# Performance work log

Hardware: AMD Instinct MI355X
Metric: run time of the kernel (lower is better)

## Reference

```python
import jax, jax.numpy as jnp
import numpy as np

MARGIN = 0.0
BINS = 10
ALPHA = 0.75
N = 16777216  # 2**24 pairs


def setup_inputs() -> dict:
    key = jax.random.key(0)
    k1, k2, k3 = jax.random.split(key, 3)
    output1 = jax.random.normal(k1, (N,), dtype=jnp.float32)
    output2 = jax.random.normal(k2, (N,), dtype=jnp.float32)
    target = jax.random.randint(k3, (N,), 0, 2, dtype=jnp.int64)
    return {"output1": output1, "output2": output2, "target": target}


def reference(output1, output2, target):
    dtype = output1.dtype
    t = target.astype(dtype)
    diff = output1 - output2
    # MarginRankingLoss(reduction='none'): max(0, -target*(x1-x2) + margin)
    loss = jnp.maximum(0.0, -t * diff + MARGIN)
    # gradient-norm proxy g in (0,1)
    expected_sign = 2.0 * t - 1.0
    g = jax.nn.sigmoid(-diff * expected_sign + MARGIN)
    g_norm = jnp.abs(g)
    edges = jnp.arange(BINS + 1, dtype=dtype) / BINS
    # histogram over BINS bins (fixed small loop over bins, vectorized over N)
    counts = jnp.stack([
        jnp.sum((g_norm >= edges[i]) & (g_norm < edges[i + 1]))
        for i in range(BINS)
    ]).astype(dtype)
    tot = jnp.clip(counts, 1.0)
    w = tot ** (-ALPHA)  # per-bin weight; constant wrt g in the original (.item() detaches)
    w = jax.lax.stop_gradient(w)
    bin_idx = jnp.clip(jnp.floor(g * BINS).astype(jnp.int32), 0, BINS - 1)
    sample_weights = w[bin_idx]
    return jnp.mean(loss * sample_weights)
```

## Files before the change

### kernel.cpp

```cpp
#include <hip/hip_runtime.h>

#define BINS 10
#define ALPHA 0.75f

constexpr int NB    = 2048;
constexpr int NT    = 256;
constexpr int NWV   = NT / 64;
constexpr int ITERS = 8;

__device__ constexpr float LTH[9] = {
    2.19722458f,  1.38629436f,  0.847297861f, 0.405465108f, 0.0f,
   -0.405465108f, -0.847297861f, -1.38629436f, -2.19722458f};

#define GHM_PROC(AX, BX, TX) do {                                    \
    float diff = (AX) - (BX);                                        \
    float nd   = -diff;                                              \
    bool  tt   = (TX) != 0;                                          \
    float u    = tt ? diff : nd;                                     \
    float loss = tt ? fmaxf(nd, 0.0f) : 0.0f;                        \
    cls[0] += loss;                                                  \
    _Pragma("unroll")                                                \
    for (int k = 1; k < BINS; ++k) {                                 \
      bool p = (u <= LTH[k - 1]);                                    \
      cls[k] += p ? loss : 0.0f;                                     \
      cnt[k] += (unsigned int)p;                                     \
    }                                                                \
  } while (0)

#define GHM_PROC4(AV, BV, TV) do {                                   \
    GHM_PROC((AV).x, (BV).x, (TV).x);                                \
    GHM_PROC((AV).y, (BV).y, (TV).y);                                \
    GHM_PROC((AV).z, (BV).z, (TV).z);                                \
    GHM_PROC((AV).w, (BV).w, (TV).w);                                \
  } while (0)

__device__ __forceinline__ void gl_lds16(const void* g, void* l) {
  __builtin_amdgcn_global_load_lds(
      (const __attribute__((address_space(1))) unsigned int*)g,
      (__attribute__((address_space(3))) unsigned int*)l, 16, 0, 0);
}

__global__ __launch_bounds__(NT) void ghm_pass1(
    const float* __restrict__ o1f, const float* __restrict__ o2f,
    const int* __restrict__ tgt, double* __restrict__ gls,
    unsigned int* __restrict__ gcnt, int n)
{
  const float4* o1 = reinterpret_cast<const float4*>(o1f);
  const float4* o2 = reinterpret_cast<const float4*>(o2f);
  const int4*   tg = reinterpret_cast<const int4*>(tgt);

  float        cls[BINS];
  unsigned int cnt[BINS];
#pragma unroll
  for (int b = 0; b < BINS; ++b) { cls[b] = 0.0f; cnt[b] = 0u; }

  const int lane = threadIdx.x & 63;
  const int wv   = threadIdx.x >> 6;

  __shared__ float4 La[3][NWV][64];
  __shared__ float4 Lb[3][NWV][64];
  __shared__ int4   Lt[3][NWV][64];

  if (n == NB * NT * ITERS * 4 && gridDim.x == NB) {
    const int gbase = blockIdx.x * (NT * ITERS);

#define STAGE(K, BUF) do {                                            \
      const int gi = gbase + (K) * NT + (int)threadIdx.x;             \
      gl_lds16(&o1[gi], &La[BUF][wv][0]);                             \
      gl_lds16(&o2[gi], &Lb[BUF][wv][0]);                             \
      gl_lds16(&tg[gi], &Lt[BUF][wv][0]);                             \
    } while (0)

    STAGE(0, 0);
    STAGE(1, 1);

#pragma unroll
    for (int k = 0; k < ITERS; ++k) {
      if (k == ITERS - 1) asm volatile("s_waitcnt vmcnt(0)" ::: "memory");
      else                asm volatile("s_waitcnt vmcnt(3)" ::: "memory");
      const int buf = k % 3;
      float4 a = La[buf][wv][lane];
      float4 b = Lb[buf][wv][lane];
      int4   t = Lt[buf][wv][lane];
      if (k + 2 < ITERS) { STAGE(k + 2, (k + 2) % 3); }
      GHM_PROC4(a, b, t);
    }
#undef STAGE
  } else {
    const int tid = blockIdx.x * NT + threadIdx.x;
    const int stride = gridDim.x * NT;
    const int n4 = n >> 2;
    for (int i = tid; i < n4; i += stride) {
      float4 a  = o1[i];
      float4 bb = o2[i];
      int4   t  = tg[i];
      GHM_PROC4(a, bb, t);
    }
    if (tid == 0) {
      for (int i = n4 * 4; i < n; ++i) GHM_PROC(o1f[i], o2f[i], tgt[i]);
    }
  }

  __shared__ float        s_ls[NWV][BINS];
  __shared__ unsigned int s_c [NWV][BINS];
#pragma unroll
  for (int b = 0; b < BINS; ++b) {
    float v = cls[b];
    unsigned int cv = cnt[b];
#pragma unroll
    for (int off = 32; off >= 1; off >>= 1) {
      v  += __shfl_down(v, off, 64);
      cv += __shfl_down(cv, off, 64);
    }
    if (lane == 0) { s_ls[wv][b] = v; s_c[wv][b] = cv; }
  }
  __syncthreads();
  if (threadIdx.x < BINS) {
    float v = 0.0f; unsigned int cv = 0u;
#pragma unroll
    for (int w = 0; w < NWV; ++w) { v += s_ls[w][threadIdx.x]; cv += s_c[w][threadIdx.x]; }
    atomicAdd(&gls[threadIdx.x], (double)v);
    if (cv) atomicAdd(&gcnt[threadIdx.x], cv);
  }
}

__global__ void ghm_final(const double* __restrict__ gls,
                          const unsigned int* __restrict__ gcnt,
                          float* __restrict__ out, int n)
{
  if (threadIdx.x == 0) {
    double             CLS[BINS + 1];
    unsigned long long CC [BINS + 1];
#pragma unroll
    for (int b = 0; b < BINS; ++b) { CLS[b] = gls[b]; CC[b] = gcnt[b]; }
    CLS[BINS] = 0.0; CC[BINS] = 0ull;
    CC[0] = (unsigned long long)n;

    double total = 0.0;
#pragma unroll
    for (int b = 0; b < BINS; ++b) {
      double lsb            = CLS[b] - CLS[b + 1];
      unsigned long long cb = CC[b] - CC[b + 1];
      float cf  = (float)cb;
      float tot = fmaxf(cf, 1.0f);
      float wgt = powf(tot, -ALPHA);
      total += lsb * (double)wgt;
    }
    out[0] = (float)(total / (double)n);
  }
}

extern "C" void kernel_launch(void* const* d_in, const int* in_sizes, int n_in,
                              void* d_out, int out_size, void* d_ws, size_t ws_size,
                              hipStream_t stream) {
  const float* o1  = (const float*)d_in[0];
  const float* o2  = (const float*)d_in[1];
  const int*   tgt = (const int*)d_in[2];
  float* out = (float*)d_out;
  const int n = in_sizes[0];

  double*       gls  = (double*)d_ws;
  unsigned int* gcnt = (unsigned int*)((char*)d_ws + BINS * sizeof(double));
  hipMemsetAsync(d_ws, 0, BINS * (sizeof(double) + sizeof(unsigned int)), stream);

  ghm_pass1<<<NB, NT, 0, stream>>>(o1, o2, tgt, gls, gcnt, n);
  ghm_final<<<1, 64, 0, stream>>>(gls, gcnt, out, n);
}
```

Baseline: 218.7 us.

## Replace LDS-staged global loads with register-prefetched nontemporal vector loads

Drops the triple-buffered global_load_lds staging through shared memory. The kernel now prefetches two iterations ahead into registers using nontemporal 128-bit loads, with a sched_barrier to keep the loads issued ahead of the compute. The grid doubles to 4096 blocks and iterations per thread halve to 4, keeping the fast-path size check consistent with 2^24 elements. This removes the LDS round trip and the manual vmcnt waits, at the cost of more live registers per thread and more blocks, each doing less work.

After: 259.0 us. 1.18x slower.

```diff
diff --git a/kernel.cpp b/kernel.cpp
--- a/kernel.cpp
+++ b/kernel.cpp
@@ -3,10 +3,12 @@
 #define BINS 10
 #define ALPHA 0.75f
 
-constexpr int NB    = 2048;
+constexpr int NB    = 4096;
 constexpr int NT    = 256;
-constexpr int NWV   = NT / 64;
-constexpr int ITERS = 8;
+constexpr int ITERS = 4;
+
+typedef float v4f __attribute__((ext_vector_type(4)));
+typedef int   v4i __attribute__((ext_vector_type(4)));
 
 __device__ constexpr float LTH[9] = {
     2.19722458f,  1.38629436f,  0.847297861f, 0.405465108f, 0.0f,
@@ -34,66 +36,47 @@
     GHM_PROC((AV).w, (BV).w, (TV).w);                                \
   } while (0)
 
-__device__ __forceinline__ void gl_lds16(const void* g, void* l) {
-  __builtin_amdgcn_global_load_lds(
-      (const __attribute__((address_space(1))) unsigned int*)g,
-      (__attribute__((address_space(3))) unsigned int*)l, 16, 0, 0);
-}
+__device__ __forceinline__ v4f nt4f(const v4f* p) { return __builtin_nontemporal_load(p); }
+__device__ __forceinline__ v4i nt4i(const v4i* p) { return __builtin_nontemporal_load(p); }
 
 __global__ __launch_bounds__(NT) void ghm_pass1(
     const float* __restrict__ o1f, const float* __restrict__ o2f,
     const int* __restrict__ tgt, double* __restrict__ gls,
     unsigned int* __restrict__ gcnt, int n)
 {
-  const float4* o1 = reinterpret_cast<const float4*>(o1f);
-  const float4* o2 = reinterpret_cast<const float4*>(o2f);
-  const int4*   tg = reinterpret_cast<const int4*>(tgt);
+  const v4f* o1 = reinterpret_cast<const v4f*>(o1f);
+  const v4f* o2 = reinterpret_cast<const v4f*>(o2f);
+  const v4i* tg = reinterpret_cast<const v4i*>(tgt);
 
   float        cls[BINS];
   unsigned int cnt[BINS];
 #pragma unroll
   for (int b = 0; b < BINS; ++b) { cls[b] = 0.0f; cnt[b] = 0u; }
 
-  const int lane = threadIdx.x & 63;
-  const int wv   = threadIdx.x >> 6;
-
-  __shared__ float4 La[3][NWV][64];
-  __shared__ float4 Lb[3][NWV][64];
-  __shared__ int4   Lt[3][NWV][64];
-
   if (n == NB * NT * ITERS * 4 && gridDim.x == NB) {
-    const int gbase = blockIdx.x * (NT * ITERS);
-
-#define STAGE(K, BUF) do {                                            \
-      const int gi = gbase + (K) * NT + (int)threadIdx.x;             \
-      gl_lds16(&o1[gi], &La[BUF][wv][0]);                             \
-      gl_lds16(&o2[gi], &Lb[BUF][wv][0]);                             \
-      gl_lds16(&tg[gi], &Lt[BUF][wv][0]);                             \
-    } while (0)
-
-    STAGE(0, 0);
-    STAGE(1, 1);
-
+    const int base = blockIdx.x * (NT * ITERS) + threadIdx.x;
+    v4f a0 = nt4f(o1 + base);      v4f b0 = nt4f(o2 + base);      v4i t0 = nt4i(tg + base);
+    v4f a1 = nt4f(o1 + base + NT); v4f b1 = nt4f(o2 + base + NT); v4i t1 = nt4i(tg + base + NT);
 #pragma unroll
-    for (int k = 0; k < ITERS; ++k) {
-      if (k == ITERS - 1) asm volatile("s_waitcnt vmcnt(0)" ::: "memory");
-      else                asm volatile("s_waitcnt vmcnt(3)" ::: "memory");
-      const int buf = k % 3;
-      float4 a = La[buf][wv][lane];
-      float4 b = Lb[buf][wv][lane];
-      int4   t = Lt[buf][wv][lane];
-      if (k + 2 < ITERS) { STAGE(k + 2, (k + 2) % 3); }
-      GHM_PROC4(a, b, t);
+    for (int k = 0; k < ITERS - 2; ++k) {
+      v4f a2 = nt4f(o1 + base + (k + 2) * NT);
+      v4f b2 = nt4f(o2 + base + (k + 2) * NT);
+      v4i t2 = nt4i(tg + base + (k + 2) * NT);
+      __builtin_amdgcn_sched_barrier(0);
+      GHM_PROC4(a0, b0, t0);
+      a0 = a1; b0 = b1; t0 = t1;
+      a1 = a2; b1 = b2; t1 = t2;
     }
-#undef STAGE
+    GHM_PROC4(a0, b0, t0);
+    GHM_PROC4(a1, b1, t1);
   } else {
     const int tid = blockIdx.x * NT + threadIdx.x;
     const int stride = gridDim.x * NT;
     const int n4 = n >> 2;
     for (int i = tid; i < n4; i += stride) {
-      float4 a  = o1[i];
-      float4 bb = o2[i];
-      int4   t  = tg[i];
+      v4f a  = o1[i];
+      v4f bb = o2[i];
+      v4i t  = tg[i];
       GHM_PROC4(a, bb, t);
     }
     if (tid == 0) {
@@ -101,8 +84,10 @@
     }
   }
 
-  __shared__ float        s_ls[NWV][BINS];
-  __shared__ unsigned int s_c [NWV][BINS];
+  const int lane = threadIdx.x & 63;
+  const int wv   = threadIdx.x >> 6;
+  __shared__ float        s_ls[NT / 64][BINS];
+  __shared__ unsigned int s_c [NT / 64][BINS];
 #pragma unroll
   for (int b = 0; b < BINS; ++b) {
     float v = cls[b];
@@ -118,7 +103,7 @@
   if (threadIdx.x < BINS) {
     float v = 0.0f; unsigned int cv = 0u;
 #pragma unroll
-    for (int w = 0; w < NWV; ++w) { v += s_ls[w][threadIdx.x]; cv += s_c[w][threadIdx.x]; }
+    for (int w = 0; w < NT / 64; ++w) { v += s_ls[w][threadIdx.x]; cv += s_c[w][threadIdx.x]; }
     atomicAdd(&gls[threadIdx.x], (double)v);
     if (cv) atomicAdd(&gcnt[threadIdx.x], cv);
   }
```
